# Optimization experiments

Measured on AMD Instinct MI355X. Metric: run time of the kernel, lower is better.

The kernel has to match this reference:

```python
import jax, jax.numpy as jnp
import numpy as np

EPS = 1e-6
NEG_SLOPE = 0.01  # torch LeakyReLU default

def ln(x, g, b):
    m = jnp.mean(x, axis=-1, keepdims=True)
    v = jnp.mean((x - m) ** 2, axis=-1, keepdims=True)
    return (x - m) / jnp.sqrt(v + EPS) * g + b

def leaky(x):
    return jnp.where(x >= 0, x, NEG_SLOPE * x)

def setup_inputs() -> dict:
    B, L, F, H, NH, LBL = 8, 1024, 1024, 256, 8, 4766
    key = jax.random.key(0)
    ks = jax.random.split(key, 16)
    def lin(k, i, o, s=0.03):
        kw, kb = jax.random.split(k)
        return jax.random.normal(kw, (i, o), jnp.float32) * s, jnp.zeros((o,), jnp.float32)
    w_in, b_in = lin(ks[0], F, H)
    w_h, b_h = lin(ks[1], H, H)
    a_w1, a_b1 = lin(ks[2], H, 64)
    a_w2, a_b2 = lin(ks[3], 64, NH)
    o_w1, o_b1 = lin(ks[4], NH * H, NH * H)
    o_w2, o_b2 = lin(ks[5], NH * H, LBL)
    CM = (jax.random.uniform(ks[6], (LBL, LBL)) < 0.002).astype(jnp.float32)
    CM = jnp.maximum(CM, jnp.eye(LBL, dtype=jnp.float32))
    return {
        'h_V': jax.random.normal(ks[7], (B, L, F), jnp.float32),
        'mask': jnp.ones((B, L), jnp.int32),
        'ln0_g': jnp.ones((F,), jnp.float32), 'ln0_b': jnp.zeros((F,), jnp.float32),
        'w_in': w_in, 'b_in': b_in,
        'ln1_g': jnp.ones((H,), jnp.float32), 'ln1_b': jnp.zeros((H,), jnp.float32),
        'w_h': w_h, 'b_h': b_h,
        'ln2_g': jnp.ones((H,), jnp.float32), 'ln2_b': jnp.zeros((H,), jnp.float32),
        'a_w1': a_w1, 'a_b1': a_b1,
        'a_lng': jnp.ones((64,), jnp.float32), 'a_lnb': jnp.zeros((64,), jnp.float32),
        'a_w2': a_w2, 'a_b2': a_b2,
        'o_w1': o_w1, 'o_b1': o_b1,
        'o_lng': jnp.ones((NH * H,), jnp.float32), 'o_lnb': jnp.zeros((NH * H,), jnp.float32),
        'o_w2': o_w2, 'o_b2': o_b2,
        'CM': CM,
    }

def reference(h_V, mask, ln0_g, ln0_b, w_in, b_in, ln1_g, ln1_b, w_h, b_h,
              ln2_g, ln2_b, a_w1, a_b1, a_lng, a_lnb, a_w2, a_b2,
              o_w1, o_b1, o_lng, o_lnb, o_w2, o_b2, CM):
    B = h_V.shape[0]
    # input + hidden blocks (eval mode: dropout is identity)
    x = ln(h_V, ln0_g, ln0_b)
    x = leaky(x @ w_in + b_in)
    x = ln(x, ln1_g, ln1_b)
    x = leaky(x @ w_h + b_h)
    x = ln(x, ln2_g, ln2_b)                      # [B,L,H]
    # multi-head attention pooling over sequence
    a = leaky(x @ a_w1 + a_b1)
    a = ln(a, a_lng, a_lnb)
    a = a @ a_w2 + a_b2                          # [B,L,NH]
    a = jnp.where(mask[:, :, None] == 0, jnp.float32(-1e9), a)
    a = jax.nn.softmax(a, axis=1)
    h = jnp.einsum('blh,bld->bhd', a, x).reshape(B, -1)  # [B,NH*H]
    # output block
    h = leaky(h @ o_w1 + o_b1)
    h = ln(h, o_lng, o_lnb)
    p = jax.nn.sigmoid(h @ o_w2 + o_b2)          # [B,LBL]
    # GO-hierarchy max-product propagation (eval path)
    out = jnp.max(p[:, None, :] * CM[None, :, :], axis=-1)  # [B,LBL]
    return out.astype(jnp.float32)
```

## Files before the change

### kernel.cpp

```cpp
#include <hip/hip_runtime.h>
#include <hip/hip_bf16.h>
#include <cstdint>

#define B_   8
#define L_   1024
#define F_   1024
#define H_   256
#define NH_  8
#define LBL_ 4766
#define M_   (B_*L_)
#define OD_  (NH_*H_)
#define NCM  (LBL_*LBL_)
#define MP_EPB 16384
#define MP_NB  ((NCM + MP_EPB - 1) / MP_EPB)

typedef unsigned short u16;
typedef unsigned int   u32;
typedef __attribute__((ext_vector_type(8))) short short8;
typedef __attribute__((ext_vector_type(4))) float float4v;

#define BF16_ONES_PAIR 0x3f803f80u

__device__ __forceinline__ float bf2f(u32 u) { return __uint_as_float(u << 16); }
__device__ __forceinline__ u16 f2bf(float f) {
    u32 u = __float_as_uint(f);
    u32 r = 0x7fffu + ((u >> 16) & 1u);
    return (u16)((u + r) >> 16);
}

struct f8 { float v[8]; };

__device__ __forceinline__ float ldS(const void* p, size_t i, bool bf) {
    return bf ? bf2f(((const u16*)p)[i]) : ((const float*)p)[i];
}
__device__ __forceinline__ float4 ld4(const void* p, size_t i, bool bf) {
    if (bf) {
        uint2 u = *(const uint2*)((const u16*)p + i);
        return make_float4(bf2f(u.x & 0xffff), bf2f(u.x >> 16),
                           bf2f(u.y & 0xffff), bf2f(u.y >> 16));
    }
    return *(const float4*)((const float*)p + i);
}
__device__ __forceinline__ f8 ld8(const void* p, size_t i, bool bf) {
    f8 r;
    if (bf) {
        uint4 u = *(const uint4*)((const u16*)p + i);
        r.v[0]=bf2f(u.x&0xffff); r.v[1]=bf2f(u.x>>16);
        r.v[2]=bf2f(u.y&0xffff); r.v[3]=bf2f(u.y>>16);
        r.v[4]=bf2f(u.z&0xffff); r.v[5]=bf2f(u.z>>16);
        r.v[6]=bf2f(u.w&0xffff); r.v[7]=bf2f(u.w>>16);
    } else {
        const float* q = (const float*)p + i;
        float4 a = *(const float4*)q, b = *(const float4*)(q+4);
        r.v[0]=a.x; r.v[1]=a.y; r.v[2]=a.z; r.v[3]=a.w;
        r.v[4]=b.x; r.v[5]=b.y; r.v[6]=b.z; r.v[7]=b.w;
    }
    return r;
}

__device__ __forceinline__ float wave_sum(float v) {
    #pragma unroll
    for (int m = 1; m < 64; m <<= 1) v += __shfl_xor(v, m, 64);
    return v;
}
__device__ __forceinline__ float wave_max(float v) {
    #pragma unroll
    for (int m = 1; m < 64; m <<= 1) v = fmaxf(v, __shfl_xor(v, m, 64));
    return v;
}
__device__ __forceinline__ float blk_sum(float v, float* sh) {
    v = wave_sum(v);
    int w = threadIdx.x >> 6, nw = blockDim.x >> 6;
    if ((threadIdx.x & 63) == 0) sh[w] = v;
    __syncthreads();
    float s = sh[0];
    for (int i = 1; i < nw; ++i) s += sh[i];
    __syncthreads();
    return s;
}
__device__ __forceinline__ float blk_max(float v, float* sh) {
    v = wave_max(v);
    int w = threadIdx.x >> 6, nw = blockDim.x >> 6;
    if ((threadIdx.x & 63) == 0) sh[w] = v;
    __syncthreads();
    float s = sh[0];
    for (int i = 1; i < nw; ++i) s = fmaxf(s, sh[i]);
    __syncthreads();
    return s;
}

__global__ __launch_bounds__(256) void prep_k(const void* __restrict__ hv,
        const void* __restrict__ g0, const void* __restrict__ b0, u16* __restrict__ x0,
        const void* __restrict__ w_in, u16* __restrict__ wt1,
        const void* __restrict__ w_h,  u16* __restrict__ wt2,
        const void* __restrict__ aw1,  u16* __restrict__ wt3,
        float* __restrict__ zA, float* __restrict__ zB,
        const u32* __restrict__ probe) {
    __shared__ u16 tile[64][65];
    __shared__ float sh[4];
    bool bf = (probe[0] == BF16_ONES_PAIR);
    int blk = blockIdx.x, t = threadIdx.x;
    if (blk < M_) {
        float4 v = ld4(hv, (size_t)blk * F_ + t * 4, bf);
        float s = v.x + v.y + v.z + v.w;
        float q = v.x*v.x + v.y*v.y + v.z*v.z + v.w*v.w;
        s = blk_sum(s, sh);
        q = blk_sum(q, sh);
        float mean = s * (1.f / F_);
        float rstd = rsqrtf(q * (1.f / F_) - mean * mean + 1e-6f);
        float4 gg = ld4(g0, t * 4, bf);
        float4 bb = ld4(b0, t * 4, bf);
        u32 o0 = f2bf((v.x - mean) * rstd * gg.x + bb.x)
               | ((u32)f2bf((v.y - mean) * rstd * gg.y + bb.y) << 16);
        u32 o1 = f2bf((v.z - mean) * rstd * gg.z + bb.z)
               | ((u32)f2bf((v.w - mean) * rstd * gg.w + bb.w) << 16);
        *(uint2*)(x0 + (size_t)blk * F_ + t * 4) = make_uint2(o0, o1);
        return;
    }
    blk -= M_;
    const void* W = nullptr; u16* WT = nullptr; int K = 0, N = 0, kt = 0, nt = 0;
    if (blk < 64)      { W = w_in; WT = wt1; K = F_; N = H_; kt = blk & 15; nt = blk >> 4; }
    else if (blk < 80) { int j = blk - 64; W = w_h; WT = wt2; K = H_; N = H_; kt = j & 3; nt = j >> 2; }
    else if (blk < 84) { int j = blk - 80; W = aw1; WT = wt3; K = H_; N = 64; kt = j; nt = 0; }
    else {
        int j = blk - 84;
        if (j < 16) {
            float4* p = (float4*)zA;
            for (int i = j * 256 + t; i < 8192; i += 4096) p[i] = make_float4(0,0,0,0);
        } else {
            j -= 16;
            float4* p = (float4*)zB;
            for (int i = j * 256 + t; i < 13628; i += 4096) p[i] = make_float4(0,0,0,0);
        }
        return;
    }
    int kt0 = kt * 64, nt0 = nt * 64;
    int r = t >> 2, cq = (t & 3) * 16;
    #pragma unroll
    for (int j = 0; j < 4; ++j) {
        float4 v = ld4(W, (size_t)(kt0 + r) * N + nt0 + cq + j * 4, bf);
        tile[r][cq + j*4 + 0] = f2bf(v.x);
        tile[r][cq + j*4 + 1] = f2bf(v.y);
        tile[r][cq + j*4 + 2] = f2bf(v.z);
        tile[r][cq + j*4 + 3] = f2bf(v.w);
    }
    __syncthreads();
    #pragma unroll
    for (int j = 0; j < 4; ++j) {
        int k = cq + j * 4;
        u32 a0 = tile[k+0][r], a1 = tile[k+1][r], a2 = tile[k+2][r], a3 = tile[k+3][r];
        uint2 o; o.x = a0 | (a1 << 16); o.y = a2 | (a3 << 16);
        *(uint2*)(WT + (size_t)(nt0 + r) * K + kt0 + k) = o;
    }
}

__global__ __launch_bounds__(256) void gemm_mfma(const u16* __restrict__ Ap, int amode,
        const float2* __restrict__ statin, const void* __restrict__ g,
        const void* __restrict__ bta, const u16* __restrict__ WT,
        const void* __restrict__ bias, u16* __restrict__ C,
        float* __restrict__ statout, int M, int N, int K,
        const u32* __restrict__ probe) {
    __shared__ short8 As[64][5];
    __shared__ short8 Bs[64][5];
    bool pbf = (probe[0] == BF16_ONES_PAIR);
    int t = threadIdx.x;
    int m0 = blockIdx.x * 64, n0 = blockIdx.y * 64;
    int r = t >> 2, kq = t & 3;
    int l = t & 63, w = t >> 6;
    int q = l >> 4, ml = l & 15;
    float4v acc[4];
    #pragma unroll
    for (int nt = 0; nt < 4; ++nt)
        #pragma unroll
        for (int i = 0; i < 4; ++i) acc[nt][i] = 0.f;
    float stm = 0.f, str = 1.f;
    if (amode == 1) {
        float2 st = statin[m0 + r];
        float mm = st.x * (1.f / K);
        stm = mm;
        str = rsqrtf(st.y * (1.f / K) - mm * mm + 1e-6f);
    }
    for (int k0 = 0; k0 < K; k0 += 32) {
        int kk = k0 + kq * 8;
        short8 pa;
        if (amode == 1) {
            f8 a  = ld8(Ap, (size_t)(m0 + r) * K + kk, true);
            f8 gg = ld8(g, kk, pbf);
            f8 bb = ld8(bta, kk, pbf);
            #pragma unroll
            for (int j = 0; j < 8; ++j)
                pa[j] = (short)f2bf((a.v[j] - stm) * str * gg.v[j] + bb.v[j]);
        } else {
            pa = *(const short8*)(Ap + (size_t)(m0 + r) * K + kk);
        }
        short8 pb = *(const short8*)(WT + (size_t)(n0 + r) * K + kk);
        __syncthreads();
        As[r][kq] = pa;
        Bs[r][kq] = pb;
        __syncthreads();
        short8 af = As[w * 16 + ml][q];
        #pragma unroll
        for (int nt = 0; nt < 4; ++nt)
            acc[nt] = __builtin_amdgcn_mfma_f32_16x16x32_bf16(af, Bs[nt*16 + ml][q],
                                                              acc[nt], 0, 0, 0);
    }
    float ov[4][4];
    #pragma unroll
    for (int nt = 0; nt < 4; ++nt) {
        int nn = n0 + nt * 16 + ml;
        float bv = ldS(bias, nn, pbf);
        #pragma unroll
        for (int reg = 0; reg < 4; ++reg) {
            float v = acc[nt][reg] + bv;
            v = v >= 0.f ? v : 0.01f * v;
            ov[nt][reg] = v;
            C[(size_t)(m0 + w * 16 + q * 4 + reg) * N + nn] = f2bf(v);
        }
    }
    if (statout) {
        #pragma unroll
        for (int reg = 0; reg < 4; ++reg) {
            float sv = ov[0][reg] + ov[1][reg] + ov[2][reg] + ov[3][reg];
            float qv = ov[0][reg]*ov[0][reg] + ov[1][reg]*ov[1][reg]
                     + ov[2][reg]*ov[2][reg] + ov[3][reg]*ov[3][reg];
            #pragma unroll
            for (int mk = 1; mk < 16; mk <<= 1) {
                sv += __shfl_xor(sv, mk, 64);
                qv += __shfl_xor(qv, mk, 64);
            }
            if (ml == 0) {
                int row = m0 + w * 16 + q * 4 + reg;
                atomicAdd(&statout[2 * row],     sv);
                atomicAdd(&statout[2 * row + 1], qv);
            }
        }
    }
}

__global__ __launch_bounds__(256) void attnlog_k(const u16* __restrict__ abr,
        const void* __restrict__ g, const void* __restrict__ b,
        const void* __restrict__ w2, const void* __restrict__ b2,
        const int* __restrict__ mask, float* __restrict__ lg,
        const u32* __restrict__ probe) {
    __shared__ float w2s[512];
    __shared__ float b2s[8];
    bool pbf = (probe[0] == BF16_ONES_PAIR);
    int t = threadIdx.x;
    for (int i = t; i < 512; i += 256) w2s[i] = ldS(w2, i, pbf);
    if (t < 8) b2s[t] = ldS(b2, t, pbf);
    __syncthreads();
    int l = t & 63, w = t >> 6;
    int row = blockIdx.x * 4 + w;
    float a = bf2f(abr[(size_t)row * 64 + l]);
    float s = wave_sum(a);
    float q = wave_sum(a * a);
    float m = s * (1.f / 64), var = q * (1.f / 64) - m * m;
    float val = (a - m) * rsqrtf(var + 1e-6f) * ldS(g, l, pbf) + ldS(b, l, pbf);
    float mine = 0.f;
    #pragma unroll
    for (int h = 0; h < 8; ++h) {
        float sh_ = wave_sum(val * w2s[l * 8 + h]);
        if (l == h) mine = sh_;
    }
    if (l < 8) {
        int bb = row >> 10, ll = row & 1023;
        float v = mine + b2s[l];
        if (mask[row] == 0) v = -1e9f;
        lg[((size_t)bb * NH_ + l) * L_ + ll] = v;
    }
}

__global__ __launch_bounds__(256) void softmax2_k(float* __restrict__ lg,
        const float2* __restrict__ st2, float* __restrict__ c1) {
    __shared__ float sh[4];
    int bh = blockIdx.x, t = threadIdx.x;
    int b = bh >> 3;
    size_t base = (size_t)bh * L_;
    float4 v = ((float4*)(lg + base))[t];
    float mx = blk_max(fmaxf(fmaxf(v.x, v.y), fmaxf(v.z, v.w)), sh);
    v.x = expf(v.x - mx); v.y = expf(v.y - mx);
    v.z = expf(v.z - mx); v.w = expf(v.w - mx);
    float s = blk_sum(v.x + v.y + v.z + v.w, sh);
    float inv = 1.f / s;
    float va[4] = {v.x, v.y, v.z, v.w};
    float ao[4];
    float c1p = 0.f;
    #pragma unroll
    for (int j = 0; j < 4; ++j) {
        int idx = t * 4 + j;
        float2 st = st2[(b << 10) + idx];
        float m = st.x * (1.f / 256);
        float r = rsqrtf(st.y * (1.f / 256) - m * m + 1e-6f);
        float aw = va[j] * inv * r;
        ao[j] = aw;
        c1p += aw * m;
    }
    ((float4*)(lg + base))[t] = make_float4(ao[0], ao[1], ao[2], ao[3]);
    float c = blk_sum(c1p, sh);
    if (t == 0) c1[bh] = c;
}

__global__ __launch_bounds__(256) void pool_part8_k(const float* __restrict__ lg,
        const u16* __restrict__ x2, float* __restrict__ Sp) {
    int bh = blockIdx.x, c = blockIdx.y, t = threadIdx.x;
    int b = bh >> 3, l0 = c << 7;
    const float* aw = lg + (size_t)bh * L_ + l0;
    const u16* xb = x2 + ((size_t)(b << 10) + l0) * 256;
    float acc = 0.f;
    #pragma unroll 8
    for (int i = 0; i < 128; ++i)
        acc += aw[i] * bf2f(xb[(size_t)i * 256 + t]);
    Sp[((size_t)c * 64 + bh) * 256 + t] = acc;
}

__global__ __launch_bounds__(256) void pool_comb8_k(const float* __restrict__ Sp,
        const float* __restrict__ c1, const void* __restrict__ g,
        const void* __restrict__ b, float* __restrict__ hp,
        const u32* __restrict__ probe) {
    bool pbf = (probe[0] == BF16_ONES_PAIR);
    int bh = blockIdx.x, t = threadIdx.x;
    float S = 0.f;
    #pragma unroll
    for (int c = 0; c < 8; ++c)
        S += Sp[((size_t)c * 64 + bh) * 256 + t];
    hp[(size_t)bh * 256 + t] = (S - c1[bh]) * ldS(g, t, pbf) + ldS(b, t, pbf);
}

__global__ __launch_bounds__(256) void gemv2_k(const float* __restrict__ hv,
        const void* __restrict__ W, float* __restrict__ acc, int K, int N,
        const u32* __restrict__ probe) {
    __shared__ float hs[8 * 64];
    bool bf = (probe[0] == BF16_ONES_PAIR);
    int t = threadIdx.x;
    int kb = blockIdx.y * 64;
    for (int i = t; i < 512; i += 256) {
        int r = i >> 6, k = i & 63;
        hs[i] = hv[(size_t)r * K + kb + k];
    }
    __syncthreads();
    int c0 = (blockIdx.x * 256 + t) * 2;
    if (c0 >= N) return;
    float a[8][2] = {};
    #pragma unroll 4
    for (int k = 0; k < 64; ++k) {
        float w0, w1;
        if (bf) {
            u32 u = *(const u32*)((const u16*)W + (size_t)(kb + k) * N + c0);
            w0 = bf2f(u & 0xffff); w1 = bf2f(u >> 16);
        } else {
            float2 fw = *(const float2*)((const float*)W + (size_t)(kb + k) * N + c0);
            w0 = fw.x; w1 = fw.y;
        }
        #pragma unroll
        for (int r = 0; r < 8; ++r) {
            float h = hs[(r << 6) + k];
            a[r][0] += h * w0; a[r][1] += h * w1;
        }
    }
    bool ok1 = (c0 + 1 < N);
    #pragma unroll
    for (int r = 0; r < 8; ++r) {
        atomicAdd(&acc[(size_t)r * N + c0], a[r][0]);
        if (ok1) atomicAdd(&acc[(size_t)r * N + c0 + 1], a[r][1]);
    }
}

__global__ __launch_bounds__(256) void out_ln_k(float* __restrict__ h,
        const void* __restrict__ bias, const void* __restrict__ g,
        const void* __restrict__ b, const u32* __restrict__ probe) {
    __shared__ float sh[4];
    bool bf = (probe[0] == BF16_ONES_PAIR);
    int row = blockIdx.x, t = threadIdx.x;
    float v[8];
    float s = 0.f, q = 0.f;
    #pragma unroll
    for (int i = 0; i < 8; ++i) {
        int c = t + i * 256;
        float x = h[(size_t)row * OD_ + c] + ldS(bias, c, bf);
        x = x >= 0.f ? x : 0.01f * x;
        v[i] = x; s += x; q += x * x;
    }
    s = blk_sum(s, sh) * (1.f / OD_);
    q = blk_sum(q, sh) * (1.f / OD_);
    float rstd = rsqrtf(q - s * s + 1e-6f);
    #pragma unroll
    for (int i = 0; i < 8; ++i) {
        int c = t + i * 256;
        h[(size_t)row * OD_ + c] = (v[i] - s) * rstd * ldS(g, c, bf) + ldS(b, c, bf);
    }
}

__global__ __launch_bounds__(256) void sigmoid_t_k(const float* __restrict__ acc,
        const void* __restrict__ bias, float* __restrict__ pt,
        float* __restrict__ out, const u32* __restrict__ probe) {
    bool bf = (probe[0] == BF16_ONES_PAIR);
    int c = blockIdx.x * 256 + threadIdx.x;
    if (c >= LBL_) return;
    float bv = ldS(bias, c, bf);
    float o[8];
    #pragma unroll
    for (int r = 0; r < 8; ++r) {
        float v = acc[(size_t)r * LBL_ + c] + bv;
        o[r] = 1.f / (1.f + expf(-v));
        out[(size_t)r * LBL_ + c] = 0.f;
    }
    float4* dst = (float4*)(pt + (size_t)c * 8);
    dst[0] = make_float4(o[0], o[1], o[2], o[3]);
    dst[1] = make_float4(o[4], o[5], o[6], o[7]);
}

__device__ __forceinline__ void mp_hit(u32 idx, float cmv,
        const float* __restrict__ pt, int* smax, u32 rowBase) {
    u32 i = idx / LBL_;
    u32 j = idx - i * LBL_;
    const float4* pj = (const float4*)(pt + (size_t)j * 8);
    float4 pa = pj[0], pb = pj[1];
    int base = (int)(i - rowBase) * 8;
    atomicMax(&smax[base + 0], __float_as_int(pa.x * cmv));
    atomicMax(&smax[base + 1], __float_as_int(pa.y * cmv));
    atomicMax(&smax[base + 2], __float_as_int(pa.z * cmv));
    atomicMax(&smax[base + 3], __float_as_int(pa.w * cmv));
    atomicMax(&smax[base + 4], __float_as_int(pb.x * cmv));
    atomicMax(&smax[base + 5], __float_as_int(pb.y * cmv));
    atomicMax(&smax[base + 6], __float_as_int(pb.z * cmv));
    atomicMax(&smax[base + 7], __float_as_int(pb.w * cmv));
}

__global__ __launch_bounds__(256) void maxprod3_k(const float* __restrict__ pt,
        const void* __restrict__ CM, float* __restrict__ out,
        const u32* __restrict__ probe) {
    __shared__ int smax[6 * 8];
    bool bf = (probe[0] == BF16_ONES_PAIR);
    int t = threadIdx.x;
    size_t blockStart = (size_t)blockIdx.x * MP_EPB;
    u32 rowBase = (u32)(blockStart / LBL_);
    for (int i = t; i < 48; i += 256) smax[i] = 0;
    __syncthreads();
    if (bf) {
        const u16* cm = (const u16*)CM;
        uint4 ch[8];
        size_t i0[8];
        #pragma unroll
        for (int u = 0; u < 8; ++u) {
            size_t idx0 = blockStart + ((size_t)u * 256 + t) * 8;
            i0[u] = idx0;
            ch[u] = (idx0 + 8 <= NCM) ? *(const uint4*)(cm + idx0)
                                      : make_uint4(0, 0, 0, 0);
        }
        #pragma unroll
        for (int u = 0; u < 8; ++u) {
            size_t idx0 = i0[u];
            if (idx0 + 8 <= NCM) {
                uint4 c4 = ch[u];
                if ((c4.x | c4.y | c4.z | c4.w) == 0) continue;
                u32 hw[4] = {c4.x, c4.y, c4.z, c4.w};
                #pragma unroll
                for (int d = 0; d < 4; ++d) {
                    u32 lo = hw[d] & 0xffff, hi = hw[d] >> 16;
                    if (lo) mp_hit((u32)idx0 + d*2,     bf2f(lo), pt, smax, rowBase);
                    if (hi) mp_hit((u32)idx0 + d*2 + 1, bf2f(hi), pt, smax, rowBase);
                }
            } else if (idx0 < NCM) {
                for (u32 e = 0; e < (u32)(NCM - idx0); ++e) {
                    u16 h = cm[idx0 + e];
                    if (h) mp_hit((u32)idx0 + e, bf2f(h), pt, smax, rowBase);
                }
            }
        }
    } else {
        const float* cm = (const float*)CM;
        #pragma unroll
        for (int u = 0; u < 16; ++u) {
            size_t idx0 = blockStart + ((size_t)u * 256 + t) * 4;
            if (idx0 >= NCM) continue;
            float v[4];
            if (idx0 + 4 <= NCM) {
                float4 f = *(const float4*)(cm + idx0);
                v[0] = f.x; v[1] = f.y; v[2] = f.z; v[3] = f.w;
            } else {
                v[0] = v[1] = v[2] = v[3] = 0.f;
                for (u32 e = 0; e < (u32)(NCM - idx0); ++e) v[e] = cm[idx0 + e];
            }
            if (v[0] == 0.f && v[1] == 0.f && v[2] == 0.f && v[3] == 0.f) continue;
            #pragma unroll
            for (int e = 0; e < 4; ++e)
                if (v[e] != 0.f) mp_hit((u32)idx0 + e, v[e], pt, smax, rowBase);
        }
    }
    __syncthreads();
    size_t lastIdx = blockStart + MP_EPB - 1;
    if (lastIdx >= NCM) lastIdx = NCM - 1;
    int nrows = (int)((u32)(lastIdx / LBL_) - rowBase) + 1;
    for (int s = t; s < nrows * 8; s += 256) {
        int v = smax[s];
        if (v != 0) {
            int rr = s >> 3, b = s & 7;
            atomicMax((int*)(out + (size_t)b * LBL_ + rowBase + rr), v);
        }
    }
}

extern "C" void kernel_launch(void* const* d_in, const int* in_sizes, int n_in,
                              void* d_out, int out_size, void* d_ws, size_t ws_size,
                              hipStream_t stream) {
    const void* hv   = d_in[0];
    const int* mask  = (const int*)d_in[1];
    const void* ln0g = d_in[2];
    const void* ln0b = d_in[3];
    const void* w_in = d_in[4];
    const void* b_in = d_in[5];
    const void* ln1g = d_in[6];
    const void* ln1b = d_in[7];
    const void* w_h  = d_in[8];
    const void* b_h  = d_in[9];
    const void* ln2g = d_in[10];
    const void* ln2b = d_in[11];
    const void* aw1  = d_in[12];
    const void* ab1  = d_in[13];
    const void* alng = d_in[14];
    const void* alnb = d_in[15];
    const void* aw2  = d_in[16];
    const void* ab2  = d_in[17];
    const void* ow1  = d_in[18];
    const void* ob1  = d_in[19];
    const void* olng = d_in[20];
    const void* olnb = d_in[21];
    const void* ow2  = d_in[22];
    const void* ob2  = d_in[23];
    const void* CM   = d_in[24];
    const u32* probe = (const u32*)ln0g;
    float* out = (float*)d_out;

    float* f = (float*)d_ws;
    float2* st1 = (float2*)f;
    float2* st2 = st1 + 8192;
    float* lg = f + 32768;
    float* c1 = lg + 65536;
    float* Sp = c1 + 64;
    float* hp = Sp + 131072;
    float* ha = hp + 16384;
    float* l2 = ha + 16384;
    float* pt = l2 + 38128;
    u16* x0  = (u16*)(pt + 38128);
    u16* x1  = x0 + 8388608;
    u16* x2  = x1 + 2097152;
    u16* abr = x2 + 2097152;
    u16* wt1 = abr + 524288;
    u16* wt2 = wt1 + 262144;
    u16* wt3 = wt2 + 65536;

    prep_k<<<M_ + 84 + 32, 256, 0, stream>>>(hv, ln0g, ln0b, x0,
                                             w_in, wt1, w_h, wt2, aw1, wt3,
                                             f, ha, probe);
    gemm_mfma<<<dim3(M_/64, 4), 256, 0, stream>>>(x0, 2, nullptr, nullptr, nullptr,
                                                  wt1, b_in, x1, (float*)st1,
                                                  M_, H_, F_, probe);
    gemm_mfma<<<dim3(M_/64, 4), 256, 0, stream>>>(x1, 1, st1, ln1g, ln1b,
                                                  wt2, b_h, x2, (float*)st2,
                                                  M_, H_, H_, probe);
    gemm_mfma<<<dim3(M_/64, 1), 256, 0, stream>>>(x2, 1, st2, ln2g, ln2b,
                                                  wt3, ab1, abr, nullptr,
                                                  M_, 64, H_, probe);
    attnlog_k<<<M_/4, 256, 0, stream>>>(abr, alng, alnb, aw2, ab2, mask, lg, probe);
    softmax2_k<<<B_*NH_, 256, 0, stream>>>(lg, st2, c1);
    pool_part8_k<<<dim3(B_*NH_, 8), 256, 0, stream>>>(lg, x2, Sp);
    pool_comb8_k<<<B_*NH_, 256, 0, stream>>>(Sp, c1, ln2g, ln2b, hp, probe);
    gemv2_k<<<dim3(OD_/512, 32), 256, 0, stream>>>(hp, ow1, ha, OD_, OD_, probe);
    out_ln_k<<<B_, 256, 0, stream>>>(ha, ob1, olng, olnb, probe);
    gemv2_k<<<dim3((LBL_+511)/512, 32), 256, 0, stream>>>(ha, ow2, l2, OD_, LBL_, probe);
    sigmoid_t_k<<<(LBL_+255)/256, 256, 0, stream>>>(l2, ob2, pt, out, probe);
    maxprod3_k<<<MP_NB, 256, 0, stream>>>(pt, CM, out, probe);
}
```

Measured before the change: 356.1 us.

## Fuse attention GEMM with logit head, and softmax with pooling

Adds a kernel that does the third GEMM (x2 to 64-wide attention hidden) with MFMA and keeps its output in shared memory. In the same kernel it applies LeakyReLU, the 64-wide layernorm and the 8-head projection, so the abr intermediate and a launch go away. A second kernel of 1024 threads per (batch, head) fuses softmax, the normalisation correction and the weighted pooling over the sequence. This replaces three kernels (softmax, partial pool, combine) and the Sp partial buffer. The trade-off is only 64 blocks of 1024 threads for the pooling reduction, which may limit parallelism on a large GPU.

```diff
diff --git a/kernel.cpp b/kernel.cpp
--- a/kernel.cpp
+++ b/kernel.cpp
@@ -237,93 +237,150 @@
     }
 }
 
-__global__ __launch_bounds__(256) void attnlog_k(const u16* __restrict__ abr,
-        const void* __restrict__ g, const void* __restrict__ b,
-        const void* __restrict__ w2, const void* __restrict__ b2,
+__global__ __launch_bounds__(256) void gemm3_attn_k(const u16* __restrict__ Ap,
+        const float2* __restrict__ statin, const void* __restrict__ g,
+        const void* __restrict__ bta, const u16* __restrict__ WT,
+        const void* __restrict__ bias,
+        const void* __restrict__ alng, const void* __restrict__ alnb,
+        const void* __restrict__ aw2, const void* __restrict__ ab2,
         const int* __restrict__ mask, float* __restrict__ lg,
         const u32* __restrict__ probe) {
+    __shared__ short8 As[64][5];
+    __shared__ short8 Bs[64][5];
+    __shared__ float at[64][65];
     __shared__ float w2s[512];
     __shared__ float b2s[8];
+    __shared__ float gs[64], bs[64];
     bool pbf = (probe[0] == BF16_ONES_PAIR);
+    const int K = 256;
     int t = threadIdx.x;
-    for (int i = t; i < 512; i += 256) w2s[i] = ldS(w2, i, pbf);
-    if (t < 8) b2s[t] = ldS(b2, t, pbf);
-    __syncthreads();
+    int m0 = blockIdx.x * 64;
+    int r = t >> 2, kq = t & 3;
     int l = t & 63, w = t >> 6;
-    int row = blockIdx.x * 4 + w;
-    float a = bf2f(abr[(size_t)row * 64 + l]);
-    float s = wave_sum(a);
-    float q = wave_sum(a * a);
-    float m = s * (1.f / 64), var = q * (1.f / 64) - m * m;
-    float val = (a - m) * rsqrtf(var + 1e-6f) * ldS(g, l, pbf) + ldS(b, l, pbf);
-    float mine = 0.f;
+    int q = l >> 4, ml = l & 15;
+    float4v acc[4];
+    #pragma unroll
+    for (int nt = 0; nt < 4; ++nt)
+        #pragma unroll
+        for (int i = 0; i < 4; ++i) acc[nt][i] = 0.f;
+    float2 st = statin[m0 + r];
+    float stm = st.x * (1.f / K);
+    float str = rsqrtf(st.y * (1.f / K) - stm * stm + 1e-6f);
+    for (int k0 = 0; k0 < K; k0 += 32) {
+        int kk = k0 + kq * 8;
+        f8 a  = ld8(Ap, (size_t)(m0 + r) * K + kk, true);
+        f8 gg = ld8(g, kk, pbf);
+        f8 bb = ld8(bta, kk, pbf);
+        short8 pa;
+        #pragma unroll
+        for (int j = 0; j < 8; ++j)
+            pa[j] = (short)f2bf((a.v[j] - stm) * str * gg.v[j] + bb.v[j]);
+        short8 pb = *(const short8*)(WT + (size_t)r * K + kk);
+        __syncthreads();
+        As[r][kq] = pa;
+        Bs[r][kq] = pb;
+        __syncthreads();
+        short8 af = As[w * 16 + ml][q];
+        #pragma unroll
+        for (int nt = 0; nt < 4; ++nt)
+            acc[nt] = __builtin_amdgcn_mfma_f32_16x16x32_bf16(af, Bs[nt*16 + ml][q],
+                                                              acc[nt], 0, 0, 0);
+    }
+    for (int i = t; i < 512; i += 256) w2s[i] = ldS(aw2, i, pbf);
+    if (t < 8) b2s[t] = ldS(ab2, t, pbf);
+    if (t < 64) { gs[t] = ldS(alng, t, pbf); bs[t] = ldS(alnb, t, pbf); }
+    #pragma unroll
+    for (int nt = 0; nt < 4; ++nt) {
+        int nn = nt * 16 + ml;
+        float bv = ldS(bias, nn, pbf);
+        #pragma unroll
+        for (int reg = 0; reg < 4; ++reg) {
+            float v = acc[nt][reg] + bv;
+            v = v >= 0.f ? v : 0.01f * v;
+            at[w * 16 + q * 4 + reg][nn] = v;
+        }
+    }
+    __syncthreads();
+    int row = t >> 2, s4 = t & 3;
+    float av[16];
+    float sum = 0.f, sq = 0.f;
+    #pragma unroll
+    for (int j = 0; j < 16; ++j) {
+        float v = at[row][s4 * 16 + j];
+        av[j] = v; sum += v; sq += v * v;
+    }
+    sum += __shfl_xor(sum, 1, 64); sum += __shfl_xor(sum, 2, 64);
+    sq  += __shfl_xor(sq, 1, 64);  sq  += __shfl_xor(sq, 2, 64);
+    float mr = sum * (1.f / 64);
+    float rr = rsqrtf(sq * (1.f / 64) - mr * mr + 1e-6f);
+    float val[16];
+    #pragma unroll
+    for (int j = 0; j < 16; ++j)
+        val[j] = (av[j] - mr) * rr * gs[s4 * 16 + j] + bs[s4 * 16 + j];
+    float hv[8];
     #pragma unroll
     for (int h = 0; h < 8; ++h) {
-        float sh_ = wave_sum(val * w2s[l * 8 + h]);
-        if (l == h) mine = sh_;
-    }
-    if (l < 8) {
-        int bb = row >> 10, ll = row & 1023;
-        float v = mine + b2s[l];
-        if (mask[row] == 0) v = -1e9f;
-        lg[((size_t)bb * NH_ + l) * L_ + ll] = v;
-    }
-}
-
-__global__ __launch_bounds__(256) void softmax2_k(float* __restrict__ lg,
-        const float2* __restrict__ st2, float* __restrict__ c1) {
-    __shared__ float sh[4];
-    int bh = blockIdx.x, t = threadIdx.x;
-    int b = bh >> 3;
-    size_t base = (size_t)bh * L_;
-    float4 v = ((float4*)(lg + base))[t];
-    float mx = blk_max(fmaxf(fmaxf(v.x, v.y), fmaxf(v.z, v.w)), sh);
-    v.x = expf(v.x - mx); v.y = expf(v.y - mx);
-    v.z = expf(v.z - mx); v.w = expf(v.w - mx);
-    float s = blk_sum(v.x + v.y + v.z + v.w, sh);
-    float inv = 1.f / s;
-    float va[4] = {v.x, v.y, v.z, v.w};
-    float ao[4];
-    float c1p = 0.f;
-    #pragma unroll
-    for (int j = 0; j < 4; ++j) {
-        int idx = t * 4 + j;
-        float2 st = st2[(b << 10) + idx];
-        float m = st.x * (1.f / 256);
-        float r = rsqrtf(st.y * (1.f / 256) - m * m + 1e-6f);
-        float aw = va[j] * inv * r;
-        ao[j] = aw;
-        c1p += aw * m;
-    }
-    ((float4*)(lg + base))[t] = make_float4(ao[0], ao[1], ao[2], ao[3]);
-    float c = blk_sum(c1p, sh);
-    if (t == 0) c1[bh] = c;
-}
-
-__global__ __launch_bounds__(256) void pool_part8_k(const float* __restrict__ lg,
-        const u16* __restrict__ x2, float* __restrict__ Sp) {
-    int bh = blockIdx.x, c = blockIdx.y, t = threadIdx.x;
-    int b = bh >> 3, l0 = c << 7;
-    const float* aw = lg + (size_t)bh * L_ + l0;
-    const u16* xb = x2 + ((size_t)(b << 10) + l0) * 256;
-    float acc = 0.f;
-    #pragma unroll 8
-    for (int i = 0; i < 128; ++i)
-        acc += aw[i] * bf2f(xb[(size_t)i * 256 + t]);
-    Sp[((size_t)c * 64 + bh) * 256 + t] = acc;
-}
-
-__global__ __launch_bounds__(256) void pool_comb8_k(const float* __restrict__ Sp,
-        const float* __restrict__ c1, const void* __restrict__ g,
-        const void* __restrict__ b, float* __restrict__ hp,
-        const u32* __restrict__ probe) {
+        float p = 0.f;
+        #pragma unroll
+        for (int j = 0; j < 16; ++j) p += val[j] * w2s[(s4 * 16 + j) * 8 + h];
+        p += __shfl_xor(p, 1, 64);
+        p += __shfl_xor(p, 2, 64);
+        hv[h] = p + b2s[h];
+    }
+    if (s4 == 0) {
+        int gr = m0 + row;
+        bool mz = (mask[gr] == 0);
+        int bb_ = gr >> 10, ll = gr & 1023;
+        #pragma unroll
+        for (int h = 0; h < 8; ++h) {
+            float v = mz ? -1e9f : hv[h];
+            lg[((size_t)bb_ * NH_ + h) * L_ + ll] = v;
+        }
+    }
+}
+
+__global__ __launch_bounds__(1024) void attnpool_k(const float* __restrict__ lg,
+        const float2* __restrict__ st2, const u16* __restrict__ x2,
+        const void* __restrict__ g, const void* __restrict__ b,
+        float* __restrict__ hp, const u32* __restrict__ probe) {
+    __shared__ float aw_s[1024];
+    __shared__ float part[16][256];
+    __shared__ float sh[16];
     bool pbf = (probe[0] == BF16_ONES_PAIR);
     int bh = blockIdx.x, t = threadIdx.x;
-    float S = 0.f;
-    #pragma unroll
-    for (int c = 0; c < 8; ++c)
-        S += Sp[((size_t)c * 64 + bh) * 256 + t];
-    hp[(size_t)bh * 256 + t] = (S - c1[bh]) * ldS(g, t, pbf) + ldS(b, t, pbf);
+    int bb = bh >> 3;
+    float v = lg[(size_t)bh * L_ + t];
+    float mx = blk_max(v, sh);
+    float e = expf(v - mx);
+    float s = blk_sum(e, sh);
+    float inv = 1.f / s;
+    float2 st = st2[(bb << 10) + t];
+    float m = st.x * (1.f / 256);
+    float r = rsqrtf(st.y * (1.f / 256) - m * m + 1e-6f);
+    float aw = e * inv * r;
+    aw_s[t] = aw;
+    float c1 = blk_sum(aw * m, sh);
+    int chunk = t >> 6, d0 = (t & 63) * 4;
+    const u16* xb = x2 + ((size_t)(bb << 10) + chunk * 64) * 256;
+    const float* awc = aw_s + chunk * 64;
+    float a0 = 0.f, a1 = 0.f, a2 = 0.f, a3 = 0.f;
+    #pragma unroll 8
+    for (int i = 0; i < 64; ++i) {
+        uint2 u = *(const uint2*)(xb + (size_t)i * 256 + d0);
+        float wv = awc[i];
+        a0 += wv * bf2f(u.x & 0xffff);
+        a1 += wv * bf2f(u.x >> 16);
+        a2 += wv * bf2f(u.y & 0xffff);
+        a3 += wv * bf2f(u.y >> 16);
+    }
+    *(float4*)&part[chunk][d0] = make_float4(a0, a1, a2, a3);
+    __syncthreads();
+    if (t < 256) {
+        float S = 0.f;
+        #pragma unroll
+        for (int c = 0; c < 16; ++c) S += part[c][t];
+        hp[(size_t)bh * 256 + t] = (S - c1) * ldS(g, t, pbf) + ldS(b, t, pbf);
+    }
 }
 
 __global__ __launch_bounds__(256) void gemv2_k(const float* __restrict__ hv,
@@ -558,13 +615,9 @@
     gemm_mfma<<<dim3(M_/64, 4), 256, 0, stream>>>(x1, 1, st1, ln1g, ln1b,
                                                   wt2, b_h, x2, (float*)st2,
                                                   M_, H_, H_, probe);
-    gemm_mfma<<<dim3(M_/64, 1), 256, 0, stream>>>(x2, 1, st2, ln2g, ln2b,
-                                                  wt3, ab1, abr, nullptr,
-                                                  M_, 64, H_, probe);
-    attnlog_k<<<M_/4, 256, 0, stream>>>(abr, alng, alnb, aw2, ab2, mask, lg, probe);
-    softmax2_k<<<B_*NH_, 256, 0, stream>>>(lg, st2, c1);
-    pool_part8_k<<<dim3(B_*NH_, 8), 256, 0, stream>>>(lg, x2, Sp);
-    pool_comb8_k<<<B_*NH_, 256, 0, stream>>>(Sp, c1, ln2g, ln2b, hp, probe);
+    gemm3_attn_k<<<M_/64, 256, 0, stream>>>(x2, st2, ln2g, ln2b, wt3, ab1,
+                                            alng, alnb, aw2, ab2, mask, lg, probe);
+    attnpool_k<<<B_*NH_, 1024, 0, stream>>>(lg, st2, x2, ln2g, ln2b, hp, probe);
     gemv2_k<<<dim3(OD_/512, 32), 256, 0, stream>>>(hp, ow1, ha, OD_, OD_, probe);
     out_ln_k<<<B_, 256, 0, stream>>>(ha, ob1, olng, olnb, probe);
     gemv2_k<<<dim3((LBL_+511)/512, 32), 256, 0, stream>>>(ha, ow2, l2, OD_, LBL_, probe);
```

New measurement: 353.7 us. Within noise of the previous version (-0.7%).
